# Kernel tuning notes

Hardware: AMD Instinct MI355X
Metric: run time of the kernel (lower is better)

The kernel has to match this reference:

```python
import jax, jax.numpy as jnp
import numpy as np

B, C, H, W = 8, 64, 112, 112
O, K, PAD, STRIDE = 64, 3, 1, 1
KK = K * K
OH = (H - K + 2 * PAD) // STRIDE + 1
OW = (W - K + 2 * PAD) // STRIDE + 1
L = OH * OW  # number of patches


def setup_inputs() -> dict:
    key = jax.random.key(0)
    k1, k2, k3 = jax.random.split(key, 3)
    x = jax.random.normal(k1, (B, C, H, W), dtype=jnp.float32)
    weight = jax.random.normal(k2, (O, C, K, K), dtype=jnp.float32)
    # one uniformly random kernel position to zero out, per patch (nums=1)
    mask_idx = jax.random.randint(k3, (L,), 0, KK, dtype=jnp.int32)
    return {"x": x, "weight": weight, "mask_idx": mask_idx}


def reference(x, weight, mask_idx):
    b = x.shape[0]
    # im2col: [b, C*KK, OH, OW], feature dim ordered channel-major (c, kh, kw)
    # which matches torch.nn.Unfold ordering.
    patches = jax.lax.conv_general_dilated_patches(
        x, (K, K), (STRIDE, STRIDE), ((PAD, PAD), (PAD, PAD)))
    patches = patches.reshape(b, C * KK, L)  # [b, CK, L]

    # Per-patch mask over kernel positions, tiled across channels
    # (equivalent to mask.repeat(1, in_channels) in the original).
    mask = jnp.ones((L, KK), dtype=x.dtype).at[jnp.arange(L), mask_idx].set(0.0)
    mask_full = jnp.tile(mask, (1, C))  # [L, C*KK]

    # weight.view(O, -1).t() -> [CK, O]; masking the weight rows per patch is
    # mathematically identical to masking the unfolded input per patch, which
    # avoids materializing the [L, CK, O] masked weight tensor.
    w2 = weight.reshape(O, C * KK).T  # [CK, O]
    out = jnp.einsum('bkl,lk,ko->bol', patches, mask_full, w2)  # [b, O, L]
    return out.reshape(b, O, OH, OW)
```

## Files before the change

kernel.cpp:

```cpp
#include <hip/hip_runtime.h>
#include <hip/hip_bf16.h>
#include <cstdint>

#define Bn 8
#define Cn 64
#define Hn 112
#define Wn 112
#define On 64
#define Ln (Hn * Wn)
#define HP 114
#define WP 114

typedef __attribute__((ext_vector_type(4))) float f32x4;
typedef __attribute__((ext_vector_type(8))) short bf16x8;
typedef __attribute__((ext_vector_type(4))) unsigned int u32x4;

__device__ __forceinline__ unsigned f2bf(float f) {
    unsigned u = __float_as_uint(f);
    unsigned r = 0x7fffu + ((u >> 16) & 1u);
    return (u + r) >> 16;
}

__global__ __launch_bounds__(64) void wpack_kernel(const float* __restrict__ w,
                                                   unsigned short* __restrict__ wpk) {
    int idx = blockIdx.x;
    int ki = idx & 1, of = (idx >> 1) & 3, p = idx >> 3;
    int lane = threadIdx.x;
    int o = of * 16 + (lane & 15);
    int cb = ki * 32 + (lane >> 4) * 8;
    unsigned int pk[4];
#pragma unroll
    for (int j = 0; j < 4; j++) {
        float v0 = w[((size_t)o * Cn + cb + 2 * j) * 9 + p];
        float v1 = w[((size_t)o * Cn + cb + 2 * j + 1) * 9 + p];
        pk[j] = f2bf(v0) | (f2bf(v1) << 16);
    }
    u32x4 v; v[0] = pk[0]; v[1] = pk[1]; v[2] = pk[2]; v[3] = pk[3];
    reinterpret_cast<u32x4*>(wpk)[idx * 64 + lane] = v;
}

__global__ __launch_bounds__(512) void conv_fused(const float* __restrict__ x,
                                                  const unsigned short* __restrict__ wpk,
                                                  const int* __restrict__ mask_idx,
                                                  float* __restrict__ out) {
    __shared__ char xs[4 * WP * Cn * 2];

    int b  = blockIdx.x & 7;
    int lt = blockIdx.x >> 3;
    int l0 = lt * 128;
    int oh0 = l0 / Wn;

    int tid = threadIdx.x;

    const float* xb = x + (size_t)b * Cn * Hn * Wn;
#pragma unroll
    for (int it = 0; it < 8; ++it) {
        int q = tid + it * 512;
        if (q < 4 * 8 * WP) {
            int row = q / (8 * WP);
            int rem = q - row * (8 * WP);
            int c8  = rem / WP;
            int wp  = rem - c8 * WP;
            int h = oh0 + row - 1;
            int w = wp - 1;
            bool inb = ((unsigned)h < (unsigned)Hn) & ((unsigned)w < (unsigned)Wn);
            const float* s = xb + ((size_t)(c8 * 8) * Hn + (inb ? h : 0)) * Wn + (inb ? w : 0);
            unsigned pk[4];
#pragma unroll
            for (int j = 0; j < 4; ++j) {
                float v0 = s[(size_t)(2 * j)     * (Hn * Wn)];
                float v1 = s[(size_t)(2 * j + 1) * (Hn * Wn)];
                if (!inb) { v0 = 0.f; v1 = 0.f; }
                pk[j] = f2bf(v0) | (f2bf(v1) << 16);
            }
            int qs = (row * WP + wp) * 8 + c8;
            int off = (qs * 16) ^ ((wp & 7) << 4);
            u32x4 v; v[0] = pk[0]; v[1] = pk[1]; v[2] = pk[2]; v[3] = pk[3];
            *reinterpret_cast<u32x4*>(xs + off) = v;
        }
    }

    int wave = tid >> 6, lane = tid & 63;
    int wr = wave >> 2;
    int wc = wave & 3;
    int g = lane >> 4, li = lane & 15;

    int pit0 = wc * 32 + li;
    int pit1 = pit0 + 16;
    int lg0 = l0 + pit0, lg1 = l0 + pit1;
    int oh_0 = lg0 / Wn, ow_0 = lg0 - oh_0 * Wn;
    int oh_1 = lg1 / Wn, ow_1 = lg1 - oh_1 * Wn;
    int r0 = oh_0 - oh0, r1 = oh_1 - oh0;
    int mv0 = mask_idx[lg0], mv1 = mask_idx[lg1];

    f32x4 acc[2][2] = {};
    const u32x4* wv = reinterpret_cast<const u32x4*>(wpk);
    const u32x4 vzero = {0u, 0u, 0u, 0u};

    u32x4 an[4];
#pragma unroll
    for (int f = 0; f < 4; ++f) an[f] = wv[(wr * 4 + f) * 64 + lane];

    __syncthreads();

    for (int p = 0; p < 9; ++p) {
        int dh = p / 3, dw = p - dh * 3;

        u32x4 ac[4] = {an[0], an[1], an[2], an[3]};
        if (p < 8) {
#pragma unroll
            for (int f = 0; f < 4; ++f)
                an[f] = wv[((p + 1) * 8 + wr * 4 + f) * 64 + lane];
        }
        bf16x8 af[2][2];
        af[0][0] = *reinterpret_cast<bf16x8*>(&ac[0]);
        af[0][1] = *reinterpret_cast<bf16x8*>(&ac[1]);
        af[1][0] = *reinterpret_cast<bf16x8*>(&ac[2]);
        af[1][1] = *reinterpret_cast<bf16x8*>(&ac[3]);

        int wq0 = ow_0 + dw, wq1 = ow_1 + dw;
        int ba0 = ((((r0 + dh) * WP + wq0) << 7) + (g << 4)) ^ ((wq0 & 7) << 4);
        int ba1 = ((((r1 + dh) * WP + wq1) << 7) + (g << 4)) ^ ((wq1 & 7) << 4);
        u32x4 v00 = *reinterpret_cast<const u32x4*>(xs + ba0);
        u32x4 v01 = *reinterpret_cast<const u32x4*>(xs + (ba0 ^ 64));
        u32x4 v10 = *reinterpret_cast<const u32x4*>(xs + ba1);
        u32x4 v11 = *reinterpret_cast<const u32x4*>(xs + (ba1 ^ 64));
        if (mv0 == p) { v00 = vzero; v01 = vzero; }
        if (mv1 == p) { v10 = vzero; v11 = vzero; }
        bf16x8 bf00 = *reinterpret_cast<bf16x8*>(&v00);
        bf16x8 bf01 = *reinterpret_cast<bf16x8*>(&v01);
        bf16x8 bf10 = *reinterpret_cast<bf16x8*>(&v10);
        bf16x8 bf11 = *reinterpret_cast<bf16x8*>(&v11);

#pragma unroll
        for (int mi = 0; mi < 2; mi++) {
            acc[mi][0] = __builtin_amdgcn_mfma_f32_16x16x32_bf16(af[mi][0], bf00, acc[mi][0], 0, 0, 0);
            acc[mi][0] = __builtin_amdgcn_mfma_f32_16x16x32_bf16(af[mi][1], bf01, acc[mi][0], 0, 0, 0);
            acc[mi][1] = __builtin_amdgcn_mfma_f32_16x16x32_bf16(af[mi][0], bf10, acc[mi][1], 0, 0, 0);
            acc[mi][1] = __builtin_amdgcn_mfma_f32_16x16x32_bf16(af[mi][1], bf11, acc[mi][1], 0, 0, 0);
        }
    }

#pragma unroll
    for (int mi = 0; mi < 2; mi++) {
#pragma unroll
        for (int ni = 0; ni < 2; ni++) {
            int o = wr * 32 + mi * 16 + g * 4;
            int lpix = l0 + wc * 32 + ni * 16 + li;
            float* dst = out + ((size_t)(b * On + o)) * Ln + lpix;
#pragma unroll
            for (int r = 0; r < 4; r++) dst[(size_t)r * Ln] = acc[mi][ni][r];
        }
    }
}

extern "C" void kernel_launch(void* const* d_in, const int* in_sizes, int n_in,
                              void* d_out, int out_size, void* d_ws, size_t ws_size,
                              hipStream_t stream) {
    const float* x    = (const float*)d_in[0];
    const float* w    = (const float*)d_in[1];
    const int*   mask = (const int*)d_in[2];
    float* out = (float*)d_out;

    unsigned short* wpk = (unsigned short*)d_ws;

    wpack_kernel<<<72,      64,  0, stream>>>(w, wpk);
    conv_fused  <<<Bn * 98, 512, 0, stream>>>(x, wpk, mask, out);
}
```

Measured before the change: 97.48 us.

## Switch conv MFMA to 32x32x16 tiles with double-buffered weight prefetch

Replaces the four 16x16x32 bf16 MFMA accumulators per wave with a single 32x32x16 MFMA accumulator and repacks the weight buffer to match that operand layout. Weight fragments are now prefetched two taps ahead into a double buffer, the first loads are issued before the input staging into shared memory, and the tap loop is fully unrolled. It also adds a min-blocks hint to launch bounds. The aim is fewer MFMA and LDS instructions per tap and better latency hiding, at the cost of more registers held live.

```diff
diff --git a/kernel.cpp b/kernel.cpp
--- a/kernel.cpp
+++ b/kernel.cpp
@@ -11,9 +11,10 @@
 #define HP 114
 #define WP 114
 
-typedef __attribute__((ext_vector_type(4))) float f32x4;
-typedef __attribute__((ext_vector_type(8))) short bf16x8;
-typedef __attribute__((ext_vector_type(4))) unsigned int u32x4;
+typedef __attribute__((ext_vector_type(4)))  float f32x4;
+typedef __attribute__((ext_vector_type(16))) float f32x16;
+typedef __attribute__((ext_vector_type(8)))  short bf16x8;
+typedef __attribute__((ext_vector_type(4)))  unsigned int u32x4;
 
 __device__ __forceinline__ unsigned f2bf(float f) {
     unsigned u = __float_as_uint(f);
@@ -24,11 +25,11 @@
 __global__ __launch_bounds__(64) void wpack_kernel(const float* __restrict__ w,
                                                    unsigned short* __restrict__ wpk) {
     int idx = blockIdx.x;
-    int ki = idx & 1, of = (idx >> 1) & 3, p = idx >> 3;
+    int kc = idx & 3, wr = (idx >> 2) & 1, p = idx >> 3;
     int lane = threadIdx.x;
-    int o = of * 16 + (lane & 15);
-    int cb = ki * 32 + (lane >> 4) * 8;
-    unsigned int pk[4];
+    int o  = wr * 32 + (lane & 31);
+    int cb = kc * 16 + (lane >> 5) * 8;
+    unsigned pk[4];
 #pragma unroll
     for (int j = 0; j < 4; j++) {
         float v0 = w[((size_t)o * Cn + cb + 2 * j) * 9 + p];
@@ -39,10 +40,10 @@
     reinterpret_cast<u32x4*>(wpk)[idx * 64 + lane] = v;
 }
 
-__global__ __launch_bounds__(512) void conv_fused(const float* __restrict__ x,
-                                                  const unsigned short* __restrict__ wpk,
-                                                  const int* __restrict__ mask_idx,
-                                                  float* __restrict__ out) {
+__global__ __launch_bounds__(512, 4) void conv_fused(const float* __restrict__ x,
+                                                     const unsigned short* __restrict__ wpk,
+                                                     const int* __restrict__ mask_idx,
+                                                     float* __restrict__ out) {
     __shared__ char xs[4 * WP * Cn * 2];
 
     int b  = blockIdx.x & 7;
@@ -50,7 +51,23 @@
     int l0 = lt * 128;
     int oh0 = l0 / Wn;
 
-    int tid = threadIdx.x;
+    int tid  = threadIdx.x;
+    int wave = tid >> 6, lane = tid & 63;
+    int wr = wave >> 2;
+    int wc = wave & 3;
+    int hi = lane >> 5;
+
+    int lg = l0 + wc * 32 + (lane & 31);
+    int oh = lg / Wn, ow = lg - oh * Wn;
+    int r  = oh - oh0;
+    int mv = mask_idx[lg];
+
+    const u32x4* wv = reinterpret_cast<const u32x4*>(wpk);
+    u32x4 apre[2][4];
+#pragma unroll
+    for (int kc = 0; kc < 4; ++kc) apre[0][kc] = wv[((0 * 2 + wr) * 4 + kc) * 64 + lane];
+#pragma unroll
+    for (int kc = 0; kc < 4; ++kc) apre[1][kc] = wv[((1 * 2 + wr) * 4 + kc) * 64 + lane];
 
     const float* xb = x + (size_t)b * Cn * Hn * Wn;
 #pragma unroll
@@ -80,77 +97,45 @@
         }
     }
 
-    int wave = tid >> 6, lane = tid & 63;
-    int wr = wave >> 2;
-    int wc = wave & 3;
-    int g = lane >> 4, li = lane & 15;
-
-    int pit0 = wc * 32 + li;
-    int pit1 = pit0 + 16;
-    int lg0 = l0 + pit0, lg1 = l0 + pit1;
-    int oh_0 = lg0 / Wn, ow_0 = lg0 - oh_0 * Wn;
-    int oh_1 = lg1 / Wn, ow_1 = lg1 - oh_1 * Wn;
-    int r0 = oh_0 - oh0, r1 = oh_1 - oh0;
-    int mv0 = mask_idx[lg0], mv1 = mask_idx[lg1];
-
-    f32x4 acc[2][2] = {};
-    const u32x4* wv = reinterpret_cast<const u32x4*>(wpk);
+    f32x16 acc = {};
     const u32x4 vzero = {0u, 0u, 0u, 0u};
-
-    u32x4 an[4];
-#pragma unroll
-    for (int f = 0; f < 4; ++f) an[f] = wv[(wr * 4 + f) * 64 + lane];
 
     __syncthreads();
 
+#pragma unroll
     for (int p = 0; p < 9; ++p) {
         int dh = p / 3, dw = p - dh * 3;
 
-        u32x4 ac[4] = {an[0], an[1], an[2], an[3]};
-        if (p < 8) {
+        int wq   = ow + dw;
+        int base = ((r + dh) * WP + wq) << 7;
+        int swz  = (wq & 7) << 4;
+        u32x4 bv[4];
 #pragma unroll
-            for (int f = 0; f < 4; ++f)
-                an[f] = wv[((p + 1) * 8 + wr * 4 + f) * 64 + lane];
+        for (int kc = 0; kc < 4; ++kc) {
+            int off = (base + ((2 * kc + hi) << 4)) ^ swz;
+            bv[kc] = *reinterpret_cast<const u32x4*>(xs + off);
         }
-        bf16x8 af[2][2];
-        af[0][0] = *reinterpret_cast<bf16x8*>(&ac[0]);
-        af[0][1] = *reinterpret_cast<bf16x8*>(&ac[1]);
-        af[1][0] = *reinterpret_cast<bf16x8*>(&ac[2]);
-        af[1][1] = *reinterpret_cast<bf16x8*>(&ac[3]);
-
-        int wq0 = ow_0 + dw, wq1 = ow_1 + dw;
-        int ba0 = ((((r0 + dh) * WP + wq0) << 7) + (g << 4)) ^ ((wq0 & 7) << 4);
-        int ba1 = ((((r1 + dh) * WP + wq1) << 7) + (g << 4)) ^ ((wq1 & 7) << 4);
-        u32x4 v00 = *reinterpret_cast<const u32x4*>(xs + ba0);
-        u32x4 v01 = *reinterpret_cast<const u32x4*>(xs + (ba0 ^ 64));
-        u32x4 v10 = *reinterpret_cast<const u32x4*>(xs + ba1);
-        u32x4 v11 = *reinterpret_cast<const u32x4*>(xs + (ba1 ^ 64));
-        if (mv0 == p) { v00 = vzero; v01 = vzero; }
-        if (mv1 == p) { v10 = vzero; v11 = vzero; }
-        bf16x8 bf00 = *reinterpret_cast<bf16x8*>(&v00);
-        bf16x8 bf01 = *reinterpret_cast<bf16x8*>(&v01);
-        bf16x8 bf10 = *reinterpret_cast<bf16x8*>(&v10);
-        bf16x8 bf11 = *reinterpret_cast<bf16x8*>(&v11);
+        if (mv == p) { bv[0] = vzero; bv[1] = vzero; bv[2] = vzero; bv[3] = vzero; }
 
 #pragma unroll
-        for (int mi = 0; mi < 2; mi++) {
-            acc[mi][0] = __builtin_amdgcn_mfma_f32_16x16x32_bf16(af[mi][0], bf00, acc[mi][0], 0, 0, 0);
-            acc[mi][0] = __builtin_amdgcn_mfma_f32_16x16x32_bf16(af[mi][1], bf01, acc[mi][0], 0, 0, 0);
-            acc[mi][1] = __builtin_amdgcn_mfma_f32_16x16x32_bf16(af[mi][0], bf10, acc[mi][1], 0, 0, 0);
-            acc[mi][1] = __builtin_amdgcn_mfma_f32_16x16x32_bf16(af[mi][1], bf11, acc[mi][1], 0, 0, 0);
+        for (int kc = 0; kc < 4; ++kc) {
+            bf16x8 a = *reinterpret_cast<bf16x8*>(&apre[p & 1][kc]);
+            bf16x8 bb = *reinterpret_cast<bf16x8*>(&bv[kc]);
+            acc = __builtin_amdgcn_mfma_f32_32x32x16_bf16(a, bb, acc, 0, 0, 0);
+        }
+
+        if (p < 7) {
+#pragma unroll
+            for (int kc = 0; kc < 4; ++kc)
+                apre[p & 1][kc] = wv[(((p + 2) * 2 + wr) * 4 + kc) * 64 + lane];
         }
     }
 
+    float* ob = out + (size_t)(b * On + wr * 32) * Ln + lg;
 #pragma unroll
-    for (int mi = 0; mi < 2; mi++) {
-#pragma unroll
-        for (int ni = 0; ni < 2; ni++) {
-            int o = wr * 32 + mi * 16 + g * 4;
-            int lpix = l0 + wc * 32 + ni * 16 + li;
-            float* dst = out + ((size_t)(b * On + o)) * Ln + lpix;
-#pragma unroll
-            for (int r = 0; r < 4; r++) dst[(size_t)r * Ln] = acc[mi][ni][r];
-        }
+    for (int reg = 0; reg < 16; ++reg) {
+        int orow = (reg & 3) + 8 * (reg >> 2) + 4 * hi;
+        ob[(size_t)orow * Ln] = acc[reg];
     }
 }
 
```

New measurement: 95.28 us. 1.02x faster.
